# Performance work log

Hardware: AMD Instinct MI355X
Metric: run time of the kernel (lower is better)

Reference implementation:

```python
import jax, jax.numpy as jnp
import numpy as np

B, C, L, T = 8, 512, 2048, 64

def setup_inputs() -> dict:
    key = jax.random.key(0)
    k1, k2, k3 = jax.random.split(key, 3)
    x = jax.random.normal(k1, (B, C, 1, L), dtype=jnp.float32)
    W1 = jax.random.normal(k2, (T, C), dtype=jnp.float32) * (1.0 / np.sqrt(C))
    W2 = jax.random.normal(k3, (T, C), dtype=jnp.float32) * (1.0 / np.sqrt(C))
    gamma = jnp.ones((1, 1), dtype=jnp.float32)
    ranges = 0  # unused by forward
    return {"x": x, "W1": W1, "W2": W2, "gamma": gamma, "ranges": ranges}

def reference(x, W1, W2, gamma, ranges):
    temp = x[:, :, 0, :]                                  # (B, C, L)
    q = jnp.einsum('tc,bcl->btl', W1, temp)               # conv1x1 -> (B, T, L)
    k = jnp.einsum('tc,bcl->btl', W2, temp)               # conv1x1 -> (B, T, L)
    scores = jnp.einsum('btl,btm->blm', q, k)             # Q^T K -> (B, L, L)
    attn = jax.nn.softmax(scores, axis=2)                 # softmax over last dim
    # temp @ attn^T: out[:, :, j] = sum_i attn[j, i] * temp[:, :, i]
    out = jnp.einsum('bci,bji->bcj', temp, attn)          # (B, C, L)
    out = temp + gamma[0, 0] * out                        # gamma scale + residual
    return out[:, :, None, :]                             # (B, C, 1, L)
```

## Files before the change

kernel.cpp:

```cpp
#include <hip/hip_runtime.h>
#include <cstddef>

#define BB 8
#define CC 512
#define LL 2048
#define TT 64

typedef short short8 __attribute__((ext_vector_type(8)));
typedef float floatx4 __attribute__((ext_vector_type(4)));
typedef unsigned short b16u;
typedef unsigned int u32;

static __device__ __forceinline__ unsigned f2bfu(float f) {
    unsigned u = __float_as_uint(f);
    u += 0x7fffu + ((u >> 16) & 1u);
    return u >> 16;
}
static __device__ __forceinline__ float bfu2f(unsigned h) {
    return __uint_as_float(h << 16);
}

#define MFMA16(a, b, c) __builtin_amdgcn_mfma_f32_16x16x32_bf16((a), (b), (c), 0, 0, 0)

__global__ __launch_bounds__(256) void wcvt_kernel(
    const float* __restrict__ W1, const float* __restrict__ W2,
    b16u* __restrict__ W1h, b16u* __restrict__ W1l,
    b16u* __restrict__ W2h, b16u* __restrict__ W2l)
{
    int flat = blockIdx.x * 256 + threadIdx.x;
    float4 v1 = *(const float4*)(W1 + (size_t)flat * 4);
    float4 v2 = *(const float4*)(W2 + (size_t)flat * 4);
    const float* e1 = (const float*)&v1;
    const float* e2 = (const float*)&v2;
    unsigned h1[4], l1[4], h2[4], l2[4];
#pragma unroll
    for (int k = 0; k < 4; ++k) {
        h1[k] = f2bfu(e1[k]); l1[k] = f2bfu(e1[k] - bfu2f(h1[k]));
        h2[k] = f2bfu(e2[k]); l2[k] = f2bfu(e2[k] - bfu2f(h2[k]));
    }
    uint2 a, b, c, d;
    a.x = h1[0] | (h1[1] << 16); a.y = h1[2] | (h1[3] << 16);
    b.x = l1[0] | (l1[1] << 16); b.y = l1[2] | (l1[3] << 16);
    c.x = h2[0] | (h2[1] << 16); c.y = h2[2] | (h2[3] << 16);
    d.x = l2[0] | (l2[1] << 16); d.y = l2[2] | (l2[3] << 16);
    *(uint2*)(W1h + (size_t)flat * 4) = a;
    *(uint2*)(W1l + (size_t)flat * 4) = b;
    *(uint2*)(W2h + (size_t)flat * 4) = c;
    *(uint2*)(W2l + (size_t)flat * 4) = d;
}

__global__ __launch_bounds__(256) void qkcvt_kernel(
    const float* __restrict__ x,
    const b16u* __restrict__ W1h, const b16u* __restrict__ W1l,
    const b16u* __restrict__ W2h, const b16u* __restrict__ W2l,
    b16u* __restrict__ Qt, b16u* __restrict__ Kt)
{
    __shared__ b16u Sxh[64 * 72];
    __shared__ b16u Sxl[64 * 72];
    __shared__ b16u S1h[64 * 72];
    __shared__ b16u S1l[64 * 72];
    __shared__ b16u S2h[64 * 72];
    __shared__ b16u S2l[64 * 72];
    const int b  = blockIdx.y;
    const int l0 = blockIdx.x * 64;
    const int tid = threadIdx.x;
    const int lane = tid & 63;
    const int w = tid >> 6;
    const int n16 = lane & 15;
    const int qd = lane >> 4;
    const float* xb = x + (size_t)b * CC * LL;

    const int cx = tid >> 2;
    const int sx = tid & 3;

    float4 xreg[4];
#pragma unroll
    for (int p = 0; p < 4; ++p)
        xreg[p] = *(const float4*)(xb + (size_t)cx * LL + l0 + (sx * 4 + p) * 4);

    floatx4 aq[4], ak[4];
#pragma unroll
    for (int nt = 0; nt < 4; ++nt) {
        aq[nt] = (floatx4){0.f, 0.f, 0.f, 0.f};
        ak[nt] = (floatx4){0.f, 0.f, 0.f, 0.f};
    }

    for (int c0 = 0; c0 < 512; c0 += 64) {
        __syncthreads();
#pragma unroll
        for (int p = 0; p < 4; ++p) {
            const float* e = (const float*)&xreg[p];
            int lbase = (sx * 4 + p) * 4;
#pragma unroll
            for (int k = 0; k < 4; ++k) {
                unsigned h = f2bfu(e[k]);
                unsigned lo = f2bfu(e[k] - bfu2f(h));
                Sxh[(lbase + k) * 72 + cx] = (b16u)h;
                Sxl[(lbase + k) * 72 + cx] = (b16u)lo;
            }
        }
#pragma unroll
        for (int p = 0; p < 2; ++p) {
            int flat = tid + p * 256;
            int t = flat >> 3, s8 = flat & 7;
            size_t off = (size_t)t * 512 + c0 + s8 * 8;
            *(uint4*)&S1h[t * 72 + s8 * 8] = *(const uint4*)(W1h + off);
            *(uint4*)&S1l[t * 72 + s8 * 8] = *(const uint4*)(W1l + off);
            *(uint4*)&S2h[t * 72 + s8 * 8] = *(const uint4*)(W2h + off);
            *(uint4*)&S2l[t * 72 + s8 * 8] = *(const uint4*)(W2l + off);
        }
        __syncthreads();
        if (c0 < 448) {
#pragma unroll
            for (int p = 0; p < 4; ++p)
                xreg[p] = *(const float4*)(xb + (size_t)(c0 + 64 + cx) * LL +
                                           l0 + (sx * 4 + p) * 4);
        }
#pragma unroll
        for (int kc = 0; kc < 2; ++kc) {
            const int ao = (w * 16 + n16) * 72 + kc * 32 + qd * 8;
            short8 a1h = *(const short8*)&S1h[ao];
            short8 a1l = *(const short8*)&S1l[ao];
            short8 a2h = *(const short8*)&S2h[ao];
            short8 a2l = *(const short8*)&S2l[ao];
#pragma unroll
            for (int nt = 0; nt < 4; ++nt) {
                const int bo = (nt * 16 + n16) * 72 + kc * 32 + qd * 8;
                short8 bh = *(const short8*)&Sxh[bo];
                short8 bl = *(const short8*)&Sxl[bo];
                aq[nt] = MFMA16(a1h, bh, aq[nt]);
                aq[nt] = MFMA16(a1h, bl, aq[nt]);
                aq[nt] = MFMA16(a1l, bh, aq[nt]);
                ak[nt] = MFMA16(a2h, bh, ak[nt]);
                ak[nt] = MFMA16(a2h, bl, ak[nt]);
                ak[nt] = MFMA16(a2l, bh, ak[nt]);
            }
        }
    }
#pragma unroll
    for (int nt = 0; nt < 4; ++nt) {
        int l = l0 + nt * 16 + n16;
        uint2 pq, pk;
        pq.x = f2bfu(aq[nt][0]) | (f2bfu(aq[nt][1]) << 16);
        pq.y = f2bfu(aq[nt][2]) | (f2bfu(aq[nt][3]) << 16);
        pk.x = f2bfu(ak[nt][0]) | (f2bfu(ak[nt][1]) << 16);
        pk.y = f2bfu(ak[nt][2]) | (f2bfu(ak[nt][3]) << 16);
        *(uint2*)(Qt + ((size_t)(b * 2048) + l) * 64 + w * 16 + qd * 4) = pq;
        *(uint2*)(Kt + ((size_t)(b * 2048) + l) * 64 + w * 16 + qd * 4) = pk;
    }
}

__global__ __launch_bounds__(256) void xcvt_kernel(
    const float* __restrict__ x, b16u* __restrict__ XT)
{
    size_t idx = ((size_t)blockIdx.x * 256 + threadIdx.x) * 4;
    float4 v = *(const float4*)(x + idx);
    uint2 wv;
    wv.x = f2bfu(v.x) | (f2bfu(v.y) << 16);
    wv.y = f2bfu(v.z) | (f2bfu(v.w) << 16);
    *(uint2*)(XT + idx) = wv;
}

__global__ __launch_bounds__(512, 2) void fused_kernel(
    const float* __restrict__ x, const b16u* __restrict__ XT,
    const b16u* __restrict__ Qt, const b16u* __restrict__ Kt,
    const float* __restrict__ gamma, float* __restrict__ out)
{
    __shared__ __align__(16) char smem[139264 + 256];
    b16u*  Pb = (b16u*)smem;
    float* Zw = (float*)(smem + 16384);
    float* Zf = (float*)(smem + 139264);

    const int b   = blockIdx.x & 7;
    const int j0  = (blockIdx.x >> 3) * 64;
    const int tid = threadIdx.x;
    const int lane = tid & 63;
    const int w    = tid >> 6;
    const int n16  = lane & 15;
    const int qd   = lane >> 4;
    const int wi   = w & 3;
    const int wj2  = w >> 2;

    const b16u* Qb = Qt + ((size_t)(b * LL) + j0 + wj2 * 32 + n16) * 64 + qd * 8;
    const b16u* Kb = Kt + ((size_t)(b * LL) + wi * 16 + n16) * 64 + qd * 8;
    const b16u* Vb = XT + ((size_t)(b * CC) + w * 64 + n16) * 2048 + qd * 8;

    short8 qf[2][2];
#pragma unroll
    for (int nt2 = 0; nt2 < 2; ++nt2)
#pragma unroll
        for (int kc = 0; kc < 2; ++kc)
            qf[nt2][kc] = *(const short8*)(Qb + nt2 * (16 * 64) + kc * 32);

    floatx4 acc[4][4];
#pragma unroll
    for (int mt = 0; mt < 4; ++mt)
#pragma unroll
        for (int nt = 0; nt < 4; ++nt) acc[mt][nt] = (floatx4){0.f, 0.f, 0.f, 0.f};
    float zacc[2] = {0.f, 0.f};

#define S_STEP(BUFOFF, KF)                                                     \
    {                                                                          \
        _Pragma("unroll")                                                      \
        for (int nt2 = 0; nt2 < 2; ++nt2) {                                    \
            floatx4 sacc = (floatx4){0.f, 0.f, 0.f, 0.f};                      \
            sacc = MFMA16(KF[0], qf[nt2][0], sacc);                            \
            sacc = MFMA16(KF[1], qf[nt2][1], sacc);                            \
            float p0 = __expf(sacc[0] - 20.0f);                                \
            float p1 = __expf(sacc[1] - 20.0f);                                \
            float p2 = __expf(sacc[2] - 20.0f);                                \
            float p3 = __expf(sacc[3] - 20.0f);                                \
            zacc[nt2] += (p0 + p1) + (p2 + p3);                                \
            uint2 pk;                                                          \
            pk.x = f2bfu(p0) | (f2bfu(p1) << 16);                              \
            pk.y = f2bfu(p2) | (f2bfu(p3) << 16);                              \
            int jl = wj2 * 32 + nt2 * 16 + n16;                                \
            int phys = (wi * 2 + (qd >> 1)) ^ (jl & 7);                        \
            *(uint2*)&Pb[(BUFOFF) + jl * 64 + phys * 8 + (qd & 1) * 4] = pk;   \
        }                                                                      \
    }

    short8 kf[2];
    kf[0] = *(const short8*)(Kb);
    kf[1] = *(const short8*)(Kb + 32);
    S_STEP(0, kf)
    kf[0] = *(const short8*)(Kb + 64 * 64);
    kf[1] = *(const short8*)(Kb + 64 * 64 + 32);
    __syncthreads();

    int buf = 0;
    for (int t = 0; t < 32; ++t) {
        short8 av[4][2];
#pragma unroll
        for (int mt = 0; mt < 4; ++mt)
#pragma unroll
            for (int kc = 0; kc < 2; ++kc)
                av[mt][kc] = *(const short8*)(Vb + (size_t)mt * (16 * 2048) +
                                              t * 64 + kc * 32);
        if (t < 31) {
            S_STEP((buf ^ 1) * 4096, kf)
            if (t < 30) {
                const b16u* kp = Kb + (size_t)(t + 2) * (64 * 64);
                kf[0] = *(const short8*)(kp);
                kf[1] = *(const short8*)(kp + 32);
            }
        }
        __builtin_amdgcn_s_setprio(1);
#pragma unroll
        for (int kc = 0; kc < 2; ++kc) {
            short8 bfr[4];
#pragma unroll
            for (int nt = 0; nt < 4; ++nt) {
                int phys = (kc * 4 + qd) ^ (n16 & 7);
                bfr[nt] = *(const short8*)&Pb[buf * 4096 +
                                              (nt * 16 + n16) * 64 + phys * 8];
            }
#pragma unroll
            for (int mt = 0; mt < 4; ++mt)
#pragma unroll
                for (int nt = 0; nt < 4; ++nt)
                    acc[mt][nt] = MFMA16(av[mt][kc], bfr[nt], acc[mt][nt]);
        }
        __builtin_amdgcn_s_setprio(0);
        __syncthreads();
        buf ^= 1;
    }
#undef S_STEP

#pragma unroll
    for (int nt2 = 0; nt2 < 2; ++nt2) {
        float z = zacc[nt2];
        z += __shfl_xor(z, 16);
        z += __shfl_xor(z, 32);
        if (qd == 0) Zw[w * 32 + nt2 * 16 + n16] = z;
    }
    __syncthreads();
    if (tid < 64) {
        int g2 = (tid >> 5) * 4;
        Zf[tid] = Zw[(g2 + 0) * 32 + (tid & 31)] + Zw[(g2 + 1) * 32 + (tid & 31)] +
                  Zw[(g2 + 2) * 32 + (tid & 31)] + Zw[(g2 + 3) * 32 + (tid & 31)];
    }
    __syncthreads();

    const float g = gamma[0];
    float* st = (float*)(smem + w * 17408);
#pragma unroll
    for (int nt = 0; nt < 4; ++nt) {
        float zi = g / Zf[nt * 16 + n16];
#pragma unroll
        for (int mt = 0; mt < 4; ++mt)
#pragma unroll
            for (int r = 0; r < 4; ++r)
                st[(mt * 16 + qd * 4 + r) * 68 + nt * 16 + n16] = acc[mt][nt][r] * zi;
    }
    __syncthreads();
#pragma unroll
    for (int p = 0; p < 16; ++p) {
        int rl = qd * 16 + p;
        size_t go = ((size_t)(b * CC) + w * 64 + rl) * 2048 + j0 + n16 * 4;
        float4 v = *(const float4*)&st[rl * 68 + n16 * 4];
        float4 xv = *(const float4*)(x + go);
        v.x += xv.x; v.y += xv.y; v.z += xv.z; v.w += xv.w;
        *(float4*)(out + go) = v;
    }
}

extern "C" void kernel_launch(void* const* d_in, const int* in_sizes, int n_in,
                              void* d_out, int out_size, void* d_ws, size_t ws_size,
                              hipStream_t stream)
{
    (void)in_sizes; (void)n_in; (void)out_size; (void)ws_size;
    const float* x     = (const float*)d_in[0];
    const float* W1    = (const float*)d_in[1];
    const float* W2    = (const float*)d_in[2];
    const float* gamma = (const float*)d_in[3];
    float* out = (float*)d_out;

    b16u* Qt  = (b16u*)d_ws;
    b16u* Kt  = Qt  + (size_t)BB * LL * TT;
    b16u* W1h = Kt  + (size_t)BB * LL * TT;
    b16u* W1l = W1h + (size_t)TT * CC;
    b16u* W2h = W1l + (size_t)TT * CC;
    b16u* W2l = W2h + (size_t)TT * CC;
    b16u* XT  = W2l + (size_t)TT * CC;

    wcvt_kernel <<<dim3(32),      256, 0, stream>>>(W1, W2, W1h, W1l, W2h, W2l);
    xcvt_kernel <<<dim3(8192),    256, 0, stream>>>(x, XT);
    qkcvt_kernel<<<dim3(32, BB),  256, 0, stream>>>(x, W1h, W1l, W2h, W2l, Qt, Kt);
    fused_kernel<<<dim3(256),     512, 0, stream>>>(x, XT, Qt, Kt, gamma, out);
}
```

Baseline: 189.8 us.

## Retile fused attention to 128 query columns by 256 channels with tiled V layout

Each block now covers 256 channels and 128 query positions instead of 512 channels and 64 positions. The S computation per block is shared across fewer channels but over more queries, which changes the balance between recomputing scores and reading V. The V conversion kernel now writes a tiled bf16 layout so each 64-key step reads contiguous chunks. The main loop is unrolled by two, with V and K register double-buffering and two P buffers in shared memory. Each block redoes the score/exp work for half the channels, and register pressure rises from the extra buffers.

```diff
diff --git a/kernel.cpp b/kernel.cpp
--- a/kernel.cpp
+++ b/kernel.cpp
@@ -153,12 +153,16 @@
 __global__ __launch_bounds__(256) void xcvt_kernel(
     const float* __restrict__ x, b16u* __restrict__ XT)
 {
-    size_t idx = ((size_t)blockIdx.x * 256 + threadIdx.x) * 4;
-    float4 v = *(const float4*)(x + idx);
+    int flat = blockIdx.x * 256 + threadIdx.x;
+    int i4 = flat & 15;
+    int t  = (flat >> 4) & 31;
+    int c  = (flat >> 9) & 511;
+    int b  = flat >> 18;
+    float4 v = *(const float4*)(x + ((size_t)(b * 512 + c)) * 2048 + t * 64 + i4 * 4);
     uint2 wv;
     wv.x = f2bfu(v.x) | (f2bfu(v.y) << 16);
     wv.y = f2bfu(v.z) | (f2bfu(v.w) << 16);
-    *(uint2*)(XT + idx) = wv;
+    *(uint2*)(XT + (((size_t)(b * 32) + t) * 512 + c) * 64 + i4 * 4) = wv;
 }
 
 __global__ __launch_bounds__(512, 2) void fused_kernel(
@@ -166,28 +170,31 @@
     const b16u* __restrict__ Qt, const b16u* __restrict__ Kt,
     const float* __restrict__ gamma, float* __restrict__ out)
 {
-    __shared__ __align__(16) char smem[139264 + 256];
-    b16u*  Pb = (b16u*)smem;
-    float* Zw = (float*)(smem + 16384);
+    __shared__ __align__(16) char smem[139776];
+    b16u*  Ps = (b16u*)smem;
+    float* Zw = (float*)(smem + 32768);
     float* Zf = (float*)(smem + 139264);
 
-    const int b   = blockIdx.x & 7;
-    const int j0  = (blockIdx.x >> 3) * 64;
+    const int bid = blockIdx.x;
+    const int b   = bid & 7;
+    const int c0  = ((bid >> 3) & 1) * 256;
+    const int j0  = (bid >> 4) * 128;
     const int tid = threadIdx.x;
     const int lane = tid & 63;
     const int w    = tid >> 6;
     const int n16  = lane & 15;
     const int qd   = lane >> 4;
     const int wi   = w & 3;
-    const int wj2  = w >> 2;
-
-    const b16u* Qb = Qt + ((size_t)(b * LL) + j0 + wj2 * 32 + n16) * 64 + qd * 8;
+    const int wh   = w >> 2;
+
+    const b16u* Qb = Qt + ((size_t)(b * LL) + j0 + wh * 64 + n16) * 64 + qd * 8;
     const b16u* Kb = Kt + ((size_t)(b * LL) + wi * 16 + n16) * 64 + qd * 8;
-    const b16u* Vb = XT + ((size_t)(b * CC) + w * 64 + n16) * 2048 + qd * 8;
-
-    short8 qf[2][2];
-#pragma unroll
-    for (int nt2 = 0; nt2 < 2; ++nt2)
+    const b16u* Vb = XT + (size_t)b * (32 * 512 * 64) +
+                     ((size_t)(c0 + wi * 64 + n16)) * 64 + qd * 8;
+
+    short8 qf[4][2];
+#pragma unroll
+    for (int nt2 = 0; nt2 < 4; ++nt2)
 #pragma unroll
         for (int kc = 0; kc < 2; ++kc)
             qf[nt2][kc] = *(const short8*)(Qb + nt2 * (16 * 64) + kc * 32);
@@ -197,88 +204,107 @@
     for (int mt = 0; mt < 4; ++mt)
 #pragma unroll
         for (int nt = 0; nt < 4; ++nt) acc[mt][nt] = (floatx4){0.f, 0.f, 0.f, 0.f};
-    float zacc[2] = {0.f, 0.f};
-
-#define S_STEP(BUFOFF, KF)                                                     \
-    {                                                                          \
-        _Pragma("unroll")                                                      \
-        for (int nt2 = 0; nt2 < 2; ++nt2) {                                    \
-            floatx4 sacc = (floatx4){0.f, 0.f, 0.f, 0.f};                      \
-            sacc = MFMA16(KF[0], qf[nt2][0], sacc);                            \
-            sacc = MFMA16(KF[1], qf[nt2][1], sacc);                            \
-            float p0 = __expf(sacc[0] - 20.0f);                                \
-            float p1 = __expf(sacc[1] - 20.0f);                                \
-            float p2 = __expf(sacc[2] - 20.0f);                                \
-            float p3 = __expf(sacc[3] - 20.0f);                                \
-            zacc[nt2] += (p0 + p1) + (p2 + p3);                                \
-            uint2 pk;                                                          \
-            pk.x = f2bfu(p0) | (f2bfu(p1) << 16);                              \
-            pk.y = f2bfu(p2) | (f2bfu(p3) << 16);                              \
-            int jl = wj2 * 32 + nt2 * 16 + n16;                                \
-            int phys = (wi * 2 + (qd >> 1)) ^ (jl & 7);                        \
-            *(uint2*)&Pb[(BUFOFF) + jl * 64 + phys * 8 + (qd & 1) * 4] = pk;   \
-        }                                                                      \
-    }
-
-    short8 kf[2];
-    kf[0] = *(const short8*)(Kb);
-    kf[1] = *(const short8*)(Kb + 32);
-    S_STEP(0, kf)
-    kf[0] = *(const short8*)(Kb + 64 * 64);
-    kf[1] = *(const short8*)(Kb + 64 * 64 + 32);
+    float zacc[4] = {0.f, 0.f, 0.f, 0.f};
+
+#define KLOAD(KR, T)                                                       \
+    {                                                                      \
+        const b16u* kp = Kb + (size_t)(T) * (64 * 64);                     \
+        KR[0] = *(const short8*)(kp);                                      \
+        KR[1] = *(const short8*)(kp + 32);                                 \
+    }
+
+#define VLOAD(VR, T)                                                       \
+    {                                                                      \
+        const b16u* vp = Vb + (size_t)(T) * 32768;                         \
+        _Pragma("unroll")                                                  \
+        for (int mt = 0; mt < 4; ++mt) {                                   \
+            VR[mt][0] = *(const short8*)(vp + mt * 1024);                  \
+            VR[mt][1] = *(const short8*)(vp + mt * 1024 + 32);             \
+        }                                                                  \
+    }
+
+#define SSTEP(PSOFF, KR)                                                   \
+    {                                                                      \
+        _Pragma("unroll")                                                  \
+        for (int nt2 = 0; nt2 < 4; ++nt2) {                                \
+            floatx4 sacc = (floatx4){0.f, 0.f, 0.f, 0.f};                  \
+            sacc = MFMA16(KR[0], qf[nt2][0], sacc);                        \
+            sacc = MFMA16(KR[1], qf[nt2][1], sacc);                        \
+            float p0 = __expf(sacc[0] - 20.0f);                            \
+            float p1 = __expf(sacc[1] - 20.0f);                            \
+            float p2 = __expf(sacc[2] - 20.0f);                            \
+            float p3 = __expf(sacc[3] - 20.0f);                            \
+            zacc[nt2] += (p0 + p1) + (p2 + p3);                            \
+            uint2 pk;                                                      \
+            pk.x = f2bfu(p0) | (f2bfu(p1) << 16);                          \
+            pk.y = f2bfu(p2) | (f2bfu(p3) << 16);                          \
+            int jl = wh * 64 + nt2 * 16 + n16;                             \
+            int phys = (wi * 2 + (qd >> 1)) ^ (n16 & 7);                   \
+            *(uint2*)&Ps[(PSOFF) + jl * 64 + phys * 8 + (qd & 1) * 4] = pk;\
+        }                                                                  \
+    }
+
+#define PVSTEP(PSOFF, VR)                                                  \
+    {                                                                      \
+        __builtin_amdgcn_s_setprio(1);                                     \
+        _Pragma("unroll")                                                  \
+        for (int kc = 0; kc < 2; ++kc) {                                   \
+            short8 bfr[4];                                                 \
+            _Pragma("unroll")                                              \
+            for (int nt = 0; nt < 4; ++nt) {                               \
+                int phys = (kc * 4 + qd) ^ (n16 & 7);                      \
+                bfr[nt] = *(const short8*)&Ps[(PSOFF) +                    \
+                    (wh * 64 + nt * 16 + n16) * 64 + phys * 8];            \
+            }                                                              \
+            _Pragma("unroll")                                              \
+            for (int mt = 0; mt < 4; ++mt)                                 \
+                _Pragma("unroll")                                          \
+                for (int nt = 0; nt < 4; ++nt)                             \
+                    acc[mt][nt] = MFMA16(VR[mt][kc], bfr[nt], acc[mt][nt]);\
+        }                                                                  \
+        __builtin_amdgcn_s_setprio(0);                                     \
+    }
+
+    short8 kA[2], kB[2], kT[2];
+    short8 v0[4][2], v1[4][2];
+
+    KLOAD(kT, 0)
+    VLOAD(v0, 0)
+    SSTEP(0, kT)
+    KLOAD(kA, 1)
     __syncthreads();
 
-    int buf = 0;
-    for (int t = 0; t < 32; ++t) {
-        short8 av[4][2];
-#pragma unroll
-        for (int mt = 0; mt < 4; ++mt)
-#pragma unroll
-            for (int kc = 0; kc < 2; ++kc)
-                av[mt][kc] = *(const short8*)(Vb + (size_t)mt * (16 * 2048) +
-                                              t * 64 + kc * 32);
-        if (t < 31) {
-            S_STEP((buf ^ 1) * 4096, kf)
-            if (t < 30) {
-                const b16u* kp = Kb + (size_t)(t + 2) * (64 * 64);
-                kf[0] = *(const short8*)(kp);
-                kf[1] = *(const short8*)(kp + 32);
-            }
-        }
-        __builtin_amdgcn_s_setprio(1);
-#pragma unroll
-        for (int kc = 0; kc < 2; ++kc) {
-            short8 bfr[4];
-#pragma unroll
-            for (int nt = 0; nt < 4; ++nt) {
-                int phys = (kc * 4 + qd) ^ (n16 & 7);
-                bfr[nt] = *(const short8*)&Pb[buf * 4096 +
-                                              (nt * 16 + n16) * 64 + phys * 8];
-            }
-#pragma unroll
-            for (int mt = 0; mt < 4; ++mt)
-#pragma unroll
-                for (int nt = 0; nt < 4; ++nt)
-                    acc[mt][nt] = MFMA16(av[mt][kc], bfr[nt], acc[mt][nt]);
-        }
-        __builtin_amdgcn_s_setprio(0);
+    for (int tt = 0; tt < 32; tt += 2) {
+        VLOAD(v1, tt + 1)
+        if (tt + 2 < 32) KLOAD(kB, tt + 2)
+        SSTEP(8192, kA)
+        PVSTEP(0, v0)
         __syncthreads();
-        buf ^= 1;
-    }
-#undef S_STEP
-
-#pragma unroll
-    for (int nt2 = 0; nt2 < 2; ++nt2) {
+        if (tt + 2 < 32) {
+            VLOAD(v0, tt + 2)
+            if (tt + 3 < 32) KLOAD(kA, tt + 3)
+            SSTEP(0, kB)
+        }
+        PVSTEP(8192, v1)
+        __syncthreads();
+    }
+#undef KLOAD
+#undef VLOAD
+#undef SSTEP
+#undef PVSTEP
+
+#pragma unroll
+    for (int nt2 = 0; nt2 < 4; ++nt2) {
         float z = zacc[nt2];
         z += __shfl_xor(z, 16);
         z += __shfl_xor(z, 32);
-        if (qd == 0) Zw[w * 32 + nt2 * 16 + n16] = z;
+        if (qd == 0) Zw[w * 64 + nt2 * 16 + n16] = z;
     }
     __syncthreads();
-    if (tid < 64) {
-        int g2 = (tid >> 5) * 4;
-        Zf[tid] = Zw[(g2 + 0) * 32 + (tid & 31)] + Zw[(g2 + 1) * 32 + (tid & 31)] +
-                  Zw[(g2 + 2) * 32 + (tid & 31)] + Zw[(g2 + 3) * 32 + (tid & 31)];
+    if (tid < 128) {
+        int hb = (tid >> 6) * 4;
+        Zf[tid] = Zw[(hb + 0) * 64 + (tid & 63)] + Zw[(hb + 1) * 64 + (tid & 63)] +
+                  Zw[(hb + 2) * 64 + (tid & 63)] + Zw[(hb + 3) * 64 + (tid & 63)];
     }
     __syncthreads();
 
@@ -286,7 +312,7 @@
     float* st = (float*)(smem + w * 17408);
 #pragma unroll
     for (int nt = 0; nt < 4; ++nt) {
-        float zi = g / Zf[nt * 16 + n16];
+        float zi = g / Zf[wh * 64 + nt * 16 + n16];
 #pragma unroll
         for (int mt = 0; mt < 4; ++mt)
 #pragma unroll
@@ -297,7 +323,8 @@
 #pragma unroll
     for (int p = 0; p < 16; ++p) {
         int rl = qd * 16 + p;
-        size_t go = ((size_t)(b * CC) + w * 64 + rl) * 2048 + j0 + n16 * 4;
+        int cg = c0 + wi * 64 + rl;
+        size_t go = ((size_t)(b * CC) + cg) * 2048 + j0 + wh * 64 + n16 * 4;
         float4 v = *(const float4*)&st[rl * 68 + n16 * 4];
         float4 xv = *(const float4*)(x + go);
         v.x += xv.x; v.y += xv.y; v.z += xv.z; v.w += xv.w;
```

Result: no change. 193.2 us (+1.8%).
